# Kernel tuning notes

Hardware: AMD Instinct MI355X
Metric: run time of the kernel (lower is better)

Reference implementation:

```python
import jax, jax.numpy as jnp
import numpy as np

B, T, C = 4, 2048, 1024
H = 16
D = C // H  # head_dim = 64

def setup_inputs() -> dict:
    key = jax.random.key(0)
    ks = jax.random.split(key, 5)
    scale = 0.02
    x = jax.random.normal(ks[0], (B, T, C), dtype=jnp.float32)
    # weights stored [in, out] (transpose of torch Linear layout; same math)
    Wqkv = jax.random.normal(ks[1], (C, 3 * C), dtype=jnp.float32) * scale
    bqkv = jnp.zeros((3 * C,), dtype=jnp.float32)
    Wproj = jax.random.normal(ks[2], (C, C), dtype=jnp.float32) * scale
    bproj = jnp.zeros((C,), dtype=jnp.float32)
    return {"x": x, "Wqkv": Wqkv, "bqkv": bqkv, "Wproj": Wproj, "bproj": bproj}

def reference(x, Wqkv, bqkv, Wproj, bproj):
    Bx, Tx, Cx = x.shape
    qkv = x @ Wqkv + bqkv                      # [B,T,3C]
    q, k, v = jnp.split(qkv, 3, axis=2)
    # [B,T,C] -> [B,H,T,D]
    q = q.reshape(Bx, Tx, H, D).transpose(0, 2, 1, 3)
    k = k.reshape(Bx, Tx, H, D).transpose(0, 2, 1, 3)
    v = v.reshape(Bx, Tx, H, D).transpose(0, 2, 1, 3)
    att = jnp.einsum('bhqd,bhkd->bhqk', q, k) / jnp.sqrt(jnp.float32(D))
    causal = jnp.tril(jnp.ones((Tx, Tx), dtype=bool))
    att = jnp.where(causal, att, jnp.float32(-jnp.inf))
    att = jax.nn.softmax(att, axis=-1)
    y = jnp.einsum('bhqk,bhkd->bhqd', att, v)  # [B,H,T,D]
    y = y.transpose(0, 2, 1, 3).reshape(Bx, Tx, Cx)
    return y @ Wproj + bproj
```

## Files before the change

### kernel.cpp

```cpp
#include <hip/hip_runtime.h>
#include <math.h>

#define Bb 4
#define Tt 2048
#define Cc 1024
#define Hh 16
#define Dd 64
#define QSC 0.18033688011112042f

typedef unsigned short ushort_t;
typedef __attribute__((ext_vector_type(8))) short short8;
typedef __attribute__((ext_vector_type(4))) float floatx4;

typedef unsigned int __attribute__((address_space(1))) u32_as1;
typedef unsigned int __attribute__((address_space(3))) u32_as3;

__device__ __forceinline__ void gld_lds16(const void* g, const void* lds_uniform) {
    __builtin_amdgcn_global_load_lds(
        (const u32_as1*)(unsigned long long)g,
        (u32_as3*)(unsigned int)(unsigned long long)lds_uniform,
        16, 0, 0);
}

__device__ inline ushort_t f2bf(float x) {
    unsigned int u = __float_as_uint(x);
    return (ushort_t)((u + 0x7FFFu + ((u >> 16) & 1u)) >> 16);
}

__device__ __forceinline__ void bar() {
    asm volatile("" ::: "memory");
    __builtin_amdgcn_s_barrier();
    asm volatile("" ::: "memory");
}

__global__ __launch_bounds__(256) void convert_kernel(
    const float* __restrict__ in, ushort_t* __restrict__ out, int n4)
{
    int i = blockIdx.x * 256 + threadIdx.x;
    if (i < n4) {
        float4 v = *(const float4*)&in[i * 4];
        ushort_t o[4] = {f2bf(v.x), f2bf(v.y), f2bf(v.z), f2bf(v.w)};
        *(uint2*)&out[i * 4] = *(uint2*)o;
    }
}

__global__ __launch_bounds__(256) void transpose_kernel(
    const float* __restrict__ W, ushort_t* __restrict__ Wt, int K, int N)
{
    __shared__ ushort_t Ts[16][72];
    const int n0 = blockIdx.x * 64;
    const int k0 = blockIdx.y * 16;
    const int t = threadIdx.x;
#pragma unroll
    for (int i = 0; i < 4; i++) {
        int e = t + i * 256;
        int kl = e >> 6, nl = e & 63;
        Ts[kl][nl] = f2bf(W[(size_t)(k0 + kl) * N + n0 + nl]);
    }
    __syncthreads();
    {
        int nl = t >> 2, kl4 = (t & 3) * 4;
        ushort_t o[4] = {Ts[kl4][nl], Ts[kl4 + 1][nl], Ts[kl4 + 2][nl], Ts[kl4 + 3][nl]};
        *(uint2*)&Wt[(size_t)(n0 + nl) * K + k0 + kl4] = *(uint2*)o;
    }
}

template <bool OUT_BF16, bool SCALE_Q>
__global__ __launch_bounds__(512) void gemm128_kernel(
    const ushort_t* __restrict__ A, const ushort_t* __restrict__ Bt,
    const float* __restrict__ bias, void* __restrict__ Co,
    int M, int N, int K)
{
    __shared__ __align__(16) ushort_t Ls[49152];

    const int tid = threadIdx.x;
    const int lane = tid & 63;
    const int w = tid >> 6;
    const int wm = w >> 2, wn = w & 3;
    const int l = lane & 15, q = lane >> 4;
    const int NT = K >> 6;

    const int n0 = blockIdx.x * 256;
    const int m0 = blockIdx.y * 128;

    const int ln = lane ^ (((lane >> 5) & 1) << 1);
    const ushort_t* Ag = A  + (size_t)(m0 + w * 16 + (ln >> 2)) * K + (ln & 3) * 8;
    const ushort_t* Bg = Bt + (size_t)(n0 + w * 16 + (ln >> 2)) * K + (ln & 3) * 8;

    const int swz = l * 32 + ((q * 8) ^ (((l >> 3) & 1) << 4));

    floatx4 acc[2][4][2];
#pragma unroll
    for (int qn = 0; qn < 2; qn++)
#pragma unroll
        for (int mf = 0; mf < 4; mf++)
#pragma unroll
            for (int nf = 0; nf < 2; nf++)
                acc[qn][mf][nf] = (floatx4){0.f, 0.f, 0.f, 0.f};

    short8 af[4][2], bf0[2][2], bf1[2][2];

#define STAGE_A(SLOT, T) {                                                      \
    const ushort_t* _g = Ag + (size_t)(T) * 64;                                 \
    const ushort_t* _l = &Ls[(SLOT) * 24576 + w * 1024];                        \
    gld_lds16(_g, _l);                                                          \
    gld_lds16(_g + 32, _l + 512); }
#define STAGE_B(SLOT, H, T) {                                                   \
    const ushort_t* _g = Bg + (size_t)(H) * 128 * K + (size_t)(T) * 64;         \
    const ushort_t* _l = &Ls[(SLOT) * 24576 + (1 + (H)) * 8192 + w * 1024];     \
    gld_lds16(_g, _l);                                                          \
    gld_lds16(_g + 32, _l + 512); }

#define LDA(SLOT) {                                                             \
    _Pragma("unroll") for (int mf = 0; mf < 4; mf++)                            \
    _Pragma("unroll") for (int kc = 0; kc < 2; kc++)                            \
        af[mf][kc] = *(const short8*)&Ls[(SLOT) * 24576 +                       \
            ((wm * 4 + mf) * 2 + kc) * 512 + swz]; }

#define LDB(SLOT, QN, DST) {                                                    \
    _Pragma("unroll") for (int nf = 0; nf < 2; nf++)                            \
    _Pragma("unroll") for (int kc = 0; kc < 2; kc++)                            \
        DST[nf][kc] = *(const short8*)&Ls[(SLOT) * 24576 + (1 + (QN)) * 8192 +  \
            ((wn * 2 + nf) * 2 + kc) * 512 + swz]; }

#define MM(QN, BF) {                                                            \
    __builtin_amdgcn_s_setprio(1);                                              \
    _Pragma("unroll") for (int kc = 0; kc < 2; kc++)                            \
    _Pragma("unroll") for (int mf = 0; mf < 4; mf++)                            \
    _Pragma("unroll") for (int nf = 0; nf < 2; nf++)                            \
        acc[QN][mf][nf] = __builtin_amdgcn_mfma_f32_16x16x32_bf16(              \
            af[mf][kc], BF[nf][kc], acc[QN][mf][nf], 0, 0, 0);                  \
    __builtin_amdgcn_s_setprio(0); }

#define LGKM0() asm volatile("s_waitcnt lgkmcnt(0)" ::: "memory")

    STAGE_A(0, 0); STAGE_B(0, 0, 0); STAGE_B(0, 1, 0);
    if (NT > 1) {
        STAGE_A(1, 1); STAGE_B(1, 0, 1);
        asm volatile("s_waitcnt vmcnt(4)" ::: "memory");
    } else {
        asm volatile("s_waitcnt vmcnt(0)" ::: "memory");
    }
    bar();

    for (int g = 0; g < NT; ++g) {
        const int slot = g & 1;

        LDA(slot);
        LDB(slot, 0, bf0);
        if (g + 1 < NT) STAGE_B(slot ^ 1, 1, g + 1);
        bar();
        LGKM0();
        MM(0, bf0);
        bar();

        LDB(slot, 1, bf1);
        if (g + 2 < NT) { STAGE_A(slot, g + 2); STAGE_B(slot, 0, g + 2); }
        bar();
        LGKM0();
        MM(1, bf1);
        if (g + 1 < NT) {
            if (g + 2 < NT) asm volatile("s_waitcnt vmcnt(4)" ::: "memory");
            else            asm volatile("s_waitcnt vmcnt(0)" ::: "memory");
            bar();
        }
    }

#pragma unroll
    for (int qn = 0; qn < 2; qn++)
#pragma unroll
        for (int nf = 0; nf < 2; nf++) {
            const int col = n0 + qn * 128 + wn * 32 + nf * 16 + l;
            const float bi = bias[col];
            const float sc = (SCALE_Q && col < 1024) ? QSC : 1.0f;
#pragma unroll
            for (int mf = 0; mf < 4; mf++)
#pragma unroll
                for (int r = 0; r < 4; r++) {
                    const int row = m0 + wm * 64 + mf * 16 + q * 4 + r;
                    const float v = (acc[qn][mf][nf][r] + bi) * sc;
                    if (OUT_BF16)
                        ((ushort_t*)Co)[(size_t)row * N + col] = f2bf(v);
                    else
                        ((float*)Co)[(size_t)row * N + col] = v;
                }
        }
#undef STAGE_A
#undef STAGE_B
#undef LDA
#undef LDB
#undef MM
#undef LGKM0
}

__device__ __forceinline__ int ks_swz(int I) {
    return I ^ (((I >> 8) & 1) * 0x28) ^ (((I >> 9) & 1) * 0x10);
}
__device__ __forceinline__ int vt_idx(int row, int col) {
    return row * 80 + (col ^ ((((row >> 2) ^ (row >> 4)) & 3) << 3));
}

#define KS_SLOT 4096
#define VT_SLOT 5120

__global__ __launch_bounds__(256, 2) void attn_mfma_kernel(
    const ushort_t* __restrict__ qkv, ushort_t* __restrict__ yatt)
{
    __shared__ __align__(16) ushort_t Ks[2 * KS_SLOT];
    __shared__ __align__(16) ushort_t Vt[2 * VT_SLOT];

    const int tid = threadIdx.x;
    const int lane = tid & 63;
    const int w = tid >> 6;
    const int quad = lane >> 4;
    const int l = lane & 15;

    const int bh = blockIdx.x;
    const int j = 15 - (int)blockIdx.y;
    const int q0 = j * 128;
    const int b = bh >> 4;
    const int h = bh & 15;
    const size_t base = (size_t)b * Tt * (3 * Cc);
    const int qoff = h * 64;
    const int koff = Cc + h * 64;
    const int voff = 2 * Cc + h * 64;

    short8 Qf[2][2];
#pragma unroll
    for (int mt = 0; mt < 2; mt++)
#pragma unroll
        for (int kc = 0; kc < 2; kc++)
            Qf[mt][kc] = *(const short8*)&qkv[base
                + (size_t)(q0 + mt * 64 + w * 16 + l) * (3 * Cc)
                + qoff + kc * 32 + quad * 8];

    floatx4 Oacc[2][4];
    float Lacc[2] = {0.f, 0.f};
#pragma unroll
    for (int mt = 0; mt < 2; mt++)
#pragma unroll
        for (int dt = 0; dt < 4; dt++)
            Oacc[mt][dt] = (floatx4){0.f, 0.f, 0.f, 0.f};

    const int srow = tid >> 2;
    const int sd0 = (tid & 3) * 16;
    const int knt = srow >> 4, kl = srow & 15;
    const int kc_s = sd0 >> 5;
    const int qp0 = (sd0 & 31) >> 3;
    const int pcol = 32 * (srow >> 5) + 8 * ((srow >> 2) & 3)
                   + 4 * ((srow >> 4) & 1) + (srow & 3);

    const int ntil = 2 * j + 2;

    const ushort_t* kp0 = &qkv[base + (size_t)srow * (3 * Cc) + koff + sd0];
    const ushort_t* vp0 = &qkv[base + (size_t)srow * (3 * Cc) + voff + sd0];

    const int ksw0 = ks_swz((knt * 2 + kc_s) * 512 + (qp0 * 16 + kl) * 8);
    const int ksw1 = ks_swz((knt * 2 + kc_s) * 512 + ((qp0 + 1) * 16 + kl) * 8);

    uint4 pk0 = *(const uint4*)kp0;
    uint4 pk1 = *(const uint4*)(kp0 + 8);
    uint4 pv0 = *(const uint4*)vp0;
    uint4 pv1 = *(const uint4*)(vp0 + 8);

#define WRITE_TILE(SLOT) {                                                      \
    *(uint4*)&Ks[(SLOT) * KS_SLOT + ksw0] = pk0;                                \
    *(uint4*)&Ks[(SLOT) * KS_SLOT + ksw1] = pk1;                                \
    ushort_t tv[16];                                                            \
    *(uint4*)&tv[0] = pv0;                                                      \
    *(uint4*)&tv[8] = pv1;                                                      \
    _Pragma("unroll") for (int t2 = 0; t2 < 16; t2++)                           \
        Vt[(SLOT) * VT_SLOT + vt_idx(sd0 + t2, pcol)] = tv[t2]; }

#define LOAD_TILE(KT) {                                                         \
    const size_t _off = (size_t)((KT) * 64) * (3 * Cc);                         \
    pk0 = *(const uint4*)(kp0 + _off);                                          \
    pk1 = *(const uint4*)(kp0 + _off + 8);                                      \
    pv0 = *(const uint4*)(vp0 + _off);                                          \
    pv1 = *(const uint4*)(vp0 + _off + 8); }

#define SM_PV(SV, MT) {                                                         \
    const int qrow = q0 + (MT) * 64 + (w << 4) + l;                             \
    const bool needm = (kbase + 63 > q0 + (MT) * 64 + (w << 4));                \
    float lsum = 0.f;                                                           \
    unsigned int pw[8];                                                         \
    _Pragma("unroll") for (int nt = 0; nt < 4; nt++) {                          \
        float e[4];                                                             \
        _Pragma("unroll") for (int r = 0; r < 4; r++) {                         \
            float s2 = SV[nt][r];                                               \
            if (needm && (kbase + nt * 16 + quad * 4 + r > qrow))               \
                s2 = -INFINITY;                                                 \
            e[r] = __builtin_amdgcn_exp2f(s2);                                  \
            lsum += e[r];                                                       \
        }                                                                       \
        pw[nt * 2 + 0] = __builtin_amdgcn_perm(                                 \
            __float_as_uint(e[1]), __float_as_uint(e[0]), 0x07060302u);         \
        pw[nt * 2 + 1] = __builtin_amdgcn_perm(                                 \
            __float_as_uint(e[3]), __float_as_uint(e[2]), 0x07060302u);         \
    }                                                                           \
    lsum += __shfl_xor(lsum, 16);                                               \
    lsum += __shfl_xor(lsum, 32);                                               \
    Lacc[MT] += lsum;                                                           \
    uint4 _u0; _u0.x = pw[0]; _u0.y = pw[1]; _u0.z = pw[2]; _u0.w = pw[3];      \
    uint4 _u1; _u1.x = pw[4]; _u1.y = pw[5]; _u1.z = pw[6]; _u1.w = pw[7];      \
    short8 Pa0 = __builtin_bit_cast(short8, _u0);                               \
    short8 Pa1 = __builtin_bit_cast(short8, _u1);                               \
    __builtin_amdgcn_s_setprio(1);                                              \
    _Pragma("unroll") for (int dt = 0; dt < 4; dt++) {                          \
        Oacc[MT][dt] = __builtin_amdgcn_mfma_f32_16x16x32_bf16(                 \
            Pa0, Vf[dt][0], Oacc[MT][dt], 0, 0, 0);                             \
        Oacc[MT][dt] = __builtin_amdgcn_mfma_f32_16x16x32_bf16(                 \
            Pa1, Vf[dt][1], Oacc[MT][dt], 0, 0, 0);                             \
    }                                                                           \
    __builtin_amdgcn_s_setprio(0); }

    WRITE_TILE(0);
    if (ntil > 1) LOAD_TILE(1);
    __syncthreads();

    for (int kt = 0; kt < ntil; kt++) {
        const int kbase = kt * 64;
        const int slot = kt & 1;

        short8 Vf[4][2];
#pragma unroll
        for (int dt = 0; dt < 4; dt++)
#pragma unroll
            for (int kc = 0; kc < 2; kc++)
                Vf[dt][kc] = *(const short8*)&Vt[slot * VT_SLOT
                    + vt_idx(dt * 16 + l, kc * 32 + quad * 8)];

        if (kt + 1 < ntil) {
            WRITE_TILE(slot ^ 1);
            if (kt + 2 < ntil) LOAD_TILE(kt + 2);
        }

        const int qmin0 = q0 + (w << 4);
        const bool act0 = (kbase <= qmin0 + 15);

        floatx4 S1[4], S0[4];
#pragma unroll
        for (int nt = 0; nt < 4; nt++) S1[nt] = (floatx4){0.f, 0.f, 0.f, 0.f};
        __builtin_amdgcn_s_setprio(1);
        if (act0) {
#pragma unroll
            for (int nt = 0; nt < 4; nt++) S0[nt] = (floatx4){0.f, 0.f, 0.f, 0.f};
#pragma unroll
            for (int kc = 0; kc < 2; kc++)
#pragma unroll
                for (int nt = 0; nt < 4; nt++) {
                    short8 kf = *(const short8*)&Ks[slot * KS_SLOT
                        + ks_swz((nt * 2 + kc) * 512 + lane * 8)];
                    S1[nt] = __builtin_amdgcn_mfma_f32_16x16x32_bf16(
                        kf, Qf[1][kc], S1[nt], 0, 0, 0);
                    S0[nt] = __builtin_amdgcn_mfma_f32_16x16x32_bf16(
                        kf, Qf[0][kc], S0[nt], 0, 0, 0);
                }
        } else {
#pragma unroll
            for (int kc = 0; kc < 2; kc++)
#pragma unroll
                for (int nt = 0; nt < 4; nt++) {
                    short8 kf = *(const short8*)&Ks[slot * KS_SLOT
                        + ks_swz((nt * 2 + kc) * 512 + lane * 8)];
                    S1[nt] = __builtin_amdgcn_mfma_f32_16x16x32_bf16(
                        kf, Qf[1][kc], S1[nt], 0, 0, 0);
                }
        }
        __builtin_amdgcn_s_setprio(0);

        SM_PV(S1, 1);
        if (act0) SM_PV(S0, 0);

        __syncthreads();
    }

#pragma unroll
    for (int mt = 0; mt < 2; mt++)
#pragma unroll
        for (int r = 0; r < 4; r++) {
            const float Lr = __shfl(Lacc[mt], quad * 4 + r);
            const float rl = 1.f / Lr;
            const int qrow = q0 + mt * 64 + (w << 4) + quad * 4 + r;
#pragma unroll
            for (int dt = 0; dt < 4; dt++)
                yatt[(size_t)(b * Tt + qrow) * Cc + h * 64 + dt * 16 + l] =
                    f2bf(Oacc[mt][dt][r] * rl);
        }
#undef WRITE_TILE
#undef LOAD_TILE
#undef SM_PV
}

extern "C" void kernel_launch(void* const* d_in, const int* in_sizes, int n_in,
                              void* d_out, int out_size, void* d_ws, size_t ws_size,
                              hipStream_t stream) {
    const float* x     = (const float*)d_in[0];
    const float* Wqkv  = (const float*)d_in[1];
    const float* bqkv  = (const float*)d_in[2];
    const float* Wproj = (const float*)d_in[3];
    const float* bproj = (const float*)d_in[4];
    float* out = (float*)d_out;

    ushort_t* qkvb   = (ushort_t*)d_ws;
    ushort_t* yattb  = qkvb + (size_t)8192 * 3072;
    ushort_t* xb     = yattb + (size_t)8192 * 1024;
    ushort_t* wqkvt  = xb + (size_t)8192 * 1024;
    ushort_t* wprojt = wqkvt + (size_t)3072 * 1024;

    convert_kernel<<<(8192 * 1024 / 4 + 255) / 256, 256, 0, stream>>>(x, xb, 8192 * 1024 / 4);
    transpose_kernel<<<dim3(3072 / 64, 1024 / 16), 256, 0, stream>>>(Wqkv, wqkvt, 1024, 3072);
    transpose_kernel<<<dim3(1024 / 64, 1024 / 16), 256, 0, stream>>>(Wproj, wprojt, 1024, 1024);

    gemm128_kernel<true, true><<<dim3(3072 / 256, 8192 / 128), 512, 0, stream>>>(
        xb, wqkvt, bqkv, qkvb, 8192, 3072, 1024);
    attn_mfma_kernel<<<dim3(64, 16), 256, 0, stream>>>(qkvb, yattb);
    gemm128_kernel<false, false><<<dim3(1024 / 256, 8192 / 128), 512, 0, stream>>>(
        yattb, wprojt, bproj, out, 8192, 1024, 1024);
}
```

Baseline: 255.8 us.

## Process key tiles in pairs per barrier with doubled LDS buffering

The attention loop now handles two 64-key tiles per iteration, with four LDS slots for K and V instead of two. This halves the number of __syncthreads barriers and lets the QK MFMAs for both tiles issue back to back before softmax and PV. The costs are LDS usage rising to about 74KB per block, which may limit occupancy at 2 blocks/CU, and more registers held for twice the prefetched global loads and S accumulators.

```diff
diff --git a/kernel.cpp b/kernel.cpp
--- a/kernel.cpp
+++ b/kernel.cpp
@@ -206,8 +206,8 @@
 __global__ __launch_bounds__(256, 2) void attn_mfma_kernel(
     const ushort_t* __restrict__ qkv, ushort_t* __restrict__ yatt)
 {
-    __shared__ __align__(16) ushort_t Ks[2 * KS_SLOT];
-    __shared__ __align__(16) ushort_t Vt[2 * VT_SLOT];
+    __shared__ __align__(16) ushort_t Ks[4 * KS_SLOT];
+    __shared__ __align__(16) ushort_t Vt[4 * VT_SLOT];
 
     const int tid = threadIdx.x;
     const int lane = tid & 63;
@@ -250,7 +250,7 @@
     const int pcol = 32 * (srow >> 5) + 8 * ((srow >> 2) & 3)
                    + 4 * ((srow >> 4) & 1) + (srow & 3);
 
-    const int ntil = 2 * j + 2;
+    const int npair = j + 1;
 
     const ushort_t* kp0 = &qkv[base + (size_t)srow * (3 * Cc) + koff + sd0];
     const ushort_t* vp0 = &qkv[base + (size_t)srow * (3 * Cc) + voff + sd0];
@@ -258,37 +258,67 @@
     const int ksw0 = ks_swz((knt * 2 + kc_s) * 512 + (qp0 * 16 + kl) * 8);
     const int ksw1 = ks_swz((knt * 2 + kc_s) * 512 + ((qp0 + 1) * 16 + kl) * 8);
 
-    uint4 pk0 = *(const uint4*)kp0;
-    uint4 pk1 = *(const uint4*)(kp0 + 8);
-    uint4 pv0 = *(const uint4*)vp0;
-    uint4 pv1 = *(const uint4*)(vp0 + 8);
-
-#define WRITE_TILE(SLOT) {                                                      \
-    *(uint4*)&Ks[(SLOT) * KS_SLOT + ksw0] = pk0;                                \
-    *(uint4*)&Ks[(SLOT) * KS_SLOT + ksw1] = pk1;                                \
+    uint4 pk00, pk01, pv00, pv01;
+    uint4 pk10, pk11, pv10, pv11;
+
+#define LOAD_PAIR(P) {                                                          \
+    const size_t _o0 = (size_t)((P) * 128) * (3 * Cc);                          \
+    const size_t _o1 = _o0 + (size_t)64 * (3 * Cc);                             \
+    pk00 = *(const uint4*)(kp0 + _o0); pk01 = *(const uint4*)(kp0 + _o0 + 8);   \
+    pv00 = *(const uint4*)(vp0 + _o0); pv01 = *(const uint4*)(vp0 + _o0 + 8);   \
+    pk10 = *(const uint4*)(kp0 + _o1); pk11 = *(const uint4*)(kp0 + _o1 + 8);   \
+    pv10 = *(const uint4*)(vp0 + _o1); pv11 = *(const uint4*)(vp0 + _o1 + 8); }
+
+#define WRITE_TILE(SLOT, PK0, PK1, PV0, PV1) {                                  \
+    *(uint4*)&Ks[(SLOT) * KS_SLOT + ksw0] = PK0;                                \
+    *(uint4*)&Ks[(SLOT) * KS_SLOT + ksw1] = PK1;                                \
     ushort_t tv[16];                                                            \
-    *(uint4*)&tv[0] = pv0;                                                      \
-    *(uint4*)&tv[8] = pv1;                                                      \
+    *(uint4*)&tv[0] = PV0;                                                      \
+    *(uint4*)&tv[8] = PV1;                                                      \
     _Pragma("unroll") for (int t2 = 0; t2 < 16; t2++)                           \
         Vt[(SLOT) * VT_SLOT + vt_idx(sd0 + t2, pcol)] = tv[t2]; }
 
-#define LOAD_TILE(KT) {                                                         \
-    const size_t _off = (size_t)((KT) * 64) * (3 * Cc);                         \
-    pk0 = *(const uint4*)(kp0 + _off);                                          \
-    pk1 = *(const uint4*)(kp0 + _off + 8);                                      \
-    pv0 = *(const uint4*)(vp0 + _off);                                          \
-    pv1 = *(const uint4*)(vp0 + _off + 8); }
-
-#define SM_PV(SV, MT) {                                                         \
+#define WRITE_PAIR(SB) {                                                        \
+    WRITE_TILE((SB), pk00, pk01, pv00, pv01);                                   \
+    WRITE_TILE((SB) + 1, pk10, pk11, pv10, pv11); }
+
+#define QK(SLOT, S1, S0, ACT0) {                                                \
+    _Pragma("unroll") for (int nt = 0; nt < 4; nt++)                            \
+        S1[nt] = (floatx4){0.f, 0.f, 0.f, 0.f};                                 \
+    __builtin_amdgcn_s_setprio(1);                                              \
+    if (ACT0) {                                                                 \
+        _Pragma("unroll") for (int nt = 0; nt < 4; nt++)                        \
+            S0[nt] = (floatx4){0.f, 0.f, 0.f, 0.f};                             \
+        _Pragma("unroll") for (int kc = 0; kc < 2; kc++)                        \
+        _Pragma("unroll") for (int nt = 0; nt < 4; nt++) {                      \
+            short8 kf = *(const short8*)&Ks[(SLOT) * KS_SLOT                    \
+                + ks_swz((nt * 2 + kc) * 512 + lane * 8)];                      \
+            S1[nt] = __builtin_amdgcn_mfma_f32_16x16x32_bf16(                   \
+                kf, Qf[1][kc], S1[nt], 0, 0, 0);                                \
+            S0[nt] = __builtin_amdgcn_mfma_f32_16x16x32_bf16(                   \
+                kf, Qf[0][kc], S0[nt], 0, 0, 0);                                \
+        }                                                                       \
+    } else {                                                                    \
+        _Pragma("unroll") for (int kc = 0; kc < 2; kc++)                        \
+        _Pragma("unroll") for (int nt = 0; nt < 4; nt++) {                      \
+            short8 kf = *(const short8*)&Ks[(SLOT) * KS_SLOT                    \
+                + ks_swz((nt * 2 + kc) * 512 + lane * 8)];                      \
+            S1[nt] = __builtin_amdgcn_mfma_f32_16x16x32_bf16(                   \
+                kf, Qf[1][kc], S1[nt], 0, 0, 0);                                \
+        }                                                                       \
+    }                                                                           \
+    __builtin_amdgcn_s_setprio(0); }
+
+#define SM_PV(SV, MT, KB, VF) {                                                 \
     const int qrow = q0 + (MT) * 64 + (w << 4) + l;                             \
-    const bool needm = (kbase + 63 > q0 + (MT) * 64 + (w << 4));                \
+    const bool needm = ((KB) + 63 > q0 + (MT) * 64 + (w << 4));                 \
     float lsum = 0.f;                                                           \
     unsigned int pw[8];                                                         \
     _Pragma("unroll") for (int nt = 0; nt < 4; nt++) {                          \
         float e[4];                                                             \
         _Pragma("unroll") for (int r = 0; r < 4; r++) {                         \
             float s2 = SV[nt][r];                                               \
-            if (needm && (kbase + nt * 16 + quad * 4 + r > qrow))               \
+            if (needm && ((KB) + nt * 16 + quad * 4 + r > qrow))                \
                 s2 = -INFINITY;                                                 \
             e[r] = __builtin_amdgcn_exp2f(s2);                                  \
             lsum += e[r];                                                       \
@@ -308,69 +338,56 @@
     __builtin_amdgcn_s_setprio(1);                                              \
     _Pragma("unroll") for (int dt = 0; dt < 4; dt++) {                          \
         Oacc[MT][dt] = __builtin_amdgcn_mfma_f32_16x16x32_bf16(                 \
-            Pa0, Vf[dt][0], Oacc[MT][dt], 0, 0, 0);                             \
+            Pa0, VF[dt][0], Oacc[MT][dt], 0, 0, 0);                             \
         Oacc[MT][dt] = __builtin_amdgcn_mfma_f32_16x16x32_bf16(                 \
-            Pa1, Vf[dt][1], Oacc[MT][dt], 0, 0, 0);                             \
+            Pa1, VF[dt][1], Oacc[MT][dt], 0, 0, 0);                             \
     }                                                                           \
     __builtin_amdgcn_s_setprio(0); }
 
-    WRITE_TILE(0);
-    if (ntil > 1) LOAD_TILE(1);
+    LOAD_PAIR(0);
+    WRITE_PAIR(0);
+    if (npair > 1) LOAD_PAIR(1);
     __syncthreads();
 
-    for (int kt = 0; kt < ntil; kt++) {
-        const int kbase = kt * 64;
-        const int slot = kt & 1;
-
-        short8 Vf[4][2];
+    for (int p = 0; p < npair; ++p) {
+        const int sb = (p & 1) * 2;
+        const int kbA = p * 128;
+        const int kbB = kbA + 64;
+
+        short8 VfA[4][2];
 #pragma unroll
         for (int dt = 0; dt < 4; dt++)
 #pragma unroll
             for (int kc = 0; kc < 2; kc++)
-                Vf[dt][kc] = *(const short8*)&Vt[slot * VT_SLOT
+                VfA[dt][kc] = *(const short8*)&Vt[sb * VT_SLOT
                     + vt_idx(dt * 16 + l, kc * 32 + quad * 8)];
 
-        if (kt + 1 < ntil) {
-            WRITE_TILE(slot ^ 1);
-            if (kt + 2 < ntil) LOAD_TILE(kt + 2);
+        if (p + 1 < npair) {
+            WRITE_PAIR(sb ^ 2);
+            if (p + 2 < npair) LOAD_PAIR(p + 2);
         }
 
         const int qmin0 = q0 + (w << 4);
-        const bool act0 = (kbase <= qmin0 + 15);
-
-        floatx4 S1[4], S0[4];
-#pragma unroll
-        for (int nt = 0; nt < 4; nt++) S1[nt] = (floatx4){0.f, 0.f, 0.f, 0.f};
-        __builtin_amdgcn_s_setprio(1);
-        if (act0) {
-#pragma unroll
-            for (int nt = 0; nt < 4; nt++) S0[nt] = (floatx4){0.f, 0.f, 0.f, 0.f};
+        const bool act0A = (kbA <= qmin0 + 15);
+        const bool act0B = (kbB <= qmin0 + 15);
+
+        floatx4 S1A[4], S0A[4], S1B[4], S0B[4];
+        QK(sb,     S1A, S0A, act0A);
+        QK(sb + 1, S1B, S0B, act0B);
+
+        SM_PV(S1A, 1, kbA, VfA);
+        if (act0A) SM_PV(S0A, 0, kbA, VfA);
+
+        short8 VfB[4][2];
+#pragma unroll
+        for (int dt = 0; dt < 4; dt++)
 #pragma unroll
             for (int kc = 0; kc < 2; kc++)
-#pragma unroll
-                for (int nt = 0; nt < 4; nt++) {
-                    short8 kf = *(const short8*)&Ks[slot * KS_SLOT
-                        + ks_swz((nt * 2 + kc) * 512 + lane * 8)];
-                    S1[nt] = __builtin_amdgcn_mfma_f32_16x16x32_bf16(
-                        kf, Qf[1][kc], S1[nt], 0, 0, 0);
-                    S0[nt] = __builtin_amdgcn_mfma_f32_16x16x32_bf16(
-                        kf, Qf[0][kc], S0[nt], 0, 0, 0);
-                }
-        } else {
-#pragma unroll
-            for (int kc = 0; kc < 2; kc++)
-#pragma unroll
-                for (int nt = 0; nt < 4; nt++) {
-                    short8 kf = *(const short8*)&Ks[slot * KS_SLOT
-                        + ks_swz((nt * 2 + kc) * 512 + lane * 8)];
-                    S1[nt] = __builtin_amdgcn_mfma_f32_16x16x32_bf16(
-                        kf, Qf[1][kc], S1[nt], 0, 0, 0);
-                }
-        }
-        __builtin_amdgcn_s_setprio(0);
-
-        SM_PV(S1, 1);
-        if (act0) SM_PV(S0, 0);
+                VfB[dt][kc] = *(const short8*)&Vt[(sb + 1) * VT_SLOT
+                    + vt_idx(dt * 16 + l, kc * 32 + quad * 8)];
+
+        SM_PV(S1B, 1, kbB, VfB);
+        if (act0B) SM_PV(S0B, 0, kbB, VfB);
 
         __syncthreads();
     }
@@ -387,8 +404,10 @@
                 yatt[(size_t)(b * Tt + qrow) * Cc + h * 64 + dt * 16 + l] =
                     f2bf(Oacc[mt][dt][r] * rl);
         }
+#undef LOAD_PAIR
 #undef WRITE_TILE
-#undef LOAD_TILE
+#undef WRITE_PAIR
+#undef QK
 #undef SM_PV
 }
 
```

After: 256.2 us. Within noise of the previous version (+0.2%).
